# Kernel tuning notes

Hardware: AMD Instinct MI355X
Metric: run time of the kernel (lower is better)

Reference implementation:

```python
import jax, jax.numpy as jnp
import numpy as np

C = 1024
H = C // 64          # 16 heads
CH = 64              # head dim
NUM_BUCKETS = 32
MAX_DISTANCE = 64
REL_SCALE = float(np.sqrt(CH))  # (channels//num_heads)**0.5 = 8
EPS = 1e-5


def group_norm(x, gamma, beta, groups):
    # x: [B, C, T]
    B, Cc, T = x.shape
    xg = x.reshape(B, groups, -1)
    m = xg.mean(-1, keepdims=True)
    v = xg.var(-1, keepdims=True)
    xn = ((xg - m) * jax.lax.rsqrt(v + EPS)).reshape(B, Cc, T)
    return xn * gamma[None, :, None] + beta[None, :, None]


def conv1d(x, w, b, pad):
    # x: [B, Cin, T], w: [Cout, Cin, K]
    y = jax.lax.conv_general_dilated(x, w, (1,), [(pad, pad)],
                                     dimension_numbers=('NCH', 'OIH', 'NCH'))
    return y + b[None, :, None]


def rel_pos_bias(T, emb):
    # lucidrains RelativePositionBias, non-causal; emb: [num_buckets, H]
    pos = jnp.arange(T)
    n = pos[:, None] - pos[None, :]          # n = -(k - q) = q - k
    half = NUM_BUCKETS // 2                  # 16
    ret = (n < 0).astype(jnp.int32) * half
    n = jnp.abs(n)
    max_exact = half // 2                    # 8
    is_small = n < max_exact
    nf = jnp.maximum(n, 1).astype(jnp.float32)
    val_large = max_exact + (jnp.log(nf / max_exact)
                             / np.log(MAX_DISTANCE / max_exact)
                             * (half - max_exact)).astype(jnp.int32)
    val_large = jnp.minimum(val_large, half - 1)
    bucket = ret + jnp.where(is_small, n, val_large)  # [T, T]
    return emb[bucket].transpose(2, 0, 1)             # [H, T, T]


def setup_inputs() -> dict:
    key = jax.random.key(0)
    ks = jax.random.split(key, 20)
    B, T = 8, 1024
    s = 0.02
    return {
        'x': jax.random.normal(ks[0], (B, C, T), jnp.float32),
        # ResBlock in_layers
        'rb_gn1_g': jnp.ones((C,), jnp.float32),
        'rb_gn1_b': jnp.zeros((C,), jnp.float32),
        'rb_conv1_w': jax.random.normal(ks[1], (C, C, 3), jnp.float32) * s,
        'rb_conv1_b': jnp.zeros((C,), jnp.float32),
        # ResBlock out_layers (zero-init in original; randomized for testing)
        'rb_gn2_g': jnp.ones((C,), jnp.float32),
        'rb_gn2_b': jnp.zeros((C,), jnp.float32),
        'rb_conv2_w': jax.random.normal(ks[2], (C, C, 3), jnp.float32) * s,
        'rb_conv2_b': jnp.zeros((C,), jnp.float32),
        # outer GroupNorm(8, C)
        'norm_g': jnp.ones((C,), jnp.float32),
        'norm_b': jnp.zeros((C,), jnp.float32),
        # AttentionBlock
        'attn_gn_g': jnp.ones((C,), jnp.float32),
        'attn_gn_b': jnp.zeros((C,), jnp.float32),
        'qkv_w': jax.random.normal(ks[3], (3 * C, C, 1), jnp.float32) * s,
        'qkv_b': jnp.zeros((3 * C,), jnp.float32),
        'proj_w': jax.random.normal(ks[4], (C, C, 1), jnp.float32) * s,
        'proj_b': jnp.zeros((C,), jnp.float32),
        'rel_emb': jax.random.normal(ks[5], (NUM_BUCKETS, H), jnp.float32) * s,
    }


def reference(x, rb_gn1_g, rb_gn1_b, rb_conv1_w, rb_conv1_b,
              rb_gn2_g, rb_gn2_b, rb_conv2_w, rb_conv2_b,
              norm_g, norm_b, attn_gn_g, attn_gn_b,
              qkv_w, qkv_b, proj_w, proj_b, rel_emb):
    B, Cc, T = x.shape
    # ResBlock: GN32 -> SiLU -> conv3 -> GN32 -> SiLU -> (dropout=0) -> conv3, + skip
    h = jax.nn.silu(group_norm(x, rb_gn1_g, rb_gn1_b, 32))
    h = conv1d(h, rb_conv1_w, rb_conv1_b, 1)
    h = jax.nn.silu(group_norm(h, rb_gn2_g, rb_gn2_b, 32))
    h = conv1d(h, rb_conv2_w, rb_conv2_b, 1)
    h = x + h
    # outer GroupNorm(8)
    h = group_norm(h, norm_g, norm_b, 8)
    # AttentionBlock with relative position bias
    xin = h
    qkv = conv1d(group_norm(h, attn_gn_g, attn_gn_b, 32), qkv_w, qkv_b, 0)
    # channel layout after reshape(bs*H, 3*ch, T): [H, 3, ch]
    qkv = qkv.reshape(B, H, 3, CH, T)
    q, k, v = qkv[:, :, 0], qkv[:, :, 1], qkv[:, :, 2]
    scale = CH ** -0.25
    w = jnp.einsum('bhct,bhcs->bhts', q * scale, k * scale)
    bias = rel_pos_bias(T, rel_emb) * REL_SCALE       # [H, T, T]
    w = jax.nn.softmax((w + bias[None]).astype(jnp.float32), axis=-1).astype(w.dtype)
    a = jnp.einsum('bhts,bhcs->bhct', w, v).reshape(B, Cc, T)
    return xin + conv1d(a, proj_w, proj_b, 0)
```

## Files before the change

kernel.cpp:

```cpp
#include <hip/hip_runtime.h>

typedef __attribute__((ext_vector_type(4))) float f32x4;
typedef __attribute__((ext_vector_type(8))) __bf16 bf16x8;
typedef __attribute__((ext_vector_type(4))) unsigned short us4;
typedef __attribute__((ext_vector_type(8))) unsigned short us8;

#define DEVI static __device__ __forceinline__

DEVI unsigned short f2bf(float f){
  union { float f; unsigned u; } x; x.f = f;
  unsigned r = x.u + 0x7fffu + ((x.u >> 16) & 1u);
  return (unsigned short)(r >> 16);
}
DEVI float bf2f(unsigned short h){
  union { unsigned u; float f; } x; x.u = ((unsigned)h) << 16;
  return x.f;
}

typedef __attribute__((address_space(1))) unsigned int gu32;
typedef __attribute__((address_space(3))) unsigned int lu32;
DEVI void gll16(const void* g, void* l){
  __builtin_amdgcn_global_load_lds((gu32*)g, (lu32*)l, 16, 0, 0);
}

DEVI f32x4 mfma16(bf16x8 a, bf16x8 b, f32x4 c){
  return __builtin_amdgcn_mfma_f32_16x16x32_bf16(a, b, c, 0, 0, 0);
}

DEVI float wredsum(float v){
  #pragma unroll
  for (int m = 1; m < 64; m <<= 1) v += __shfl_xor(v, m);
  return v;
}

__global__ __launch_bounds__(256) void conv_w_prep(const float* __restrict__ w,
                                                   unsigned short* __restrict__ wp){
  int idx = blockIdx.x * 256 + threadIdx.x;
  const float* p = w + (size_t)idx * 3;
  wp[idx]           = f2bf(p[0]);
  wp[1048576 + idx] = f2bf(p[1]);
  wp[2097152 + idx] = f2bf(p[2]);
}

__global__ __launch_bounds__(256) void cast_f2b(const float* __restrict__ in,
                                                unsigned short* __restrict__ out, int n4){
  int idx = blockIdx.x * 256 + threadIdx.x;
  if (idx < n4){
    f32x4 v = *(const f32x4*)&in[(size_t)idx * 4];
    us4 o;
    #pragma unroll
    for (int j = 0; j < 4; j++) o[j] = f2bf(v[j]);
    *(us4*)&out[(size_t)idx * 4] = o;
  }
}

__global__ __launch_bounds__(256) void btab_k(const float* __restrict__ emb,
                                              float* __restrict__ btab){
  int idx = blockIdx.x * 256 + threadIdx.x;
  if (idx >= 2047 * 16) return;
  int d = idx >> 4, h = idx & 15;
  int n0 = d - 1023;
  int ret = (n0 < 0) ? 16 : 0;
  int n = (n0 < 0) ? -n0 : n0;
  int bucket;
  if (n < 8) bucket = ret + n;
  else {
    float ratio = logf((float)n * 0.125f) / 2.0794415416798357f;
    int vl = 8 + (int)(ratio * 8.0f);
    bucket = ret + (vl < 15 ? vl : 15);
  }
  btab[h * 2048 + d] = emb[bucket * 16 + h] * 11.541560327111707f;
}

__global__ __launch_bounds__(256) void zero_pads(unsigned short* __restrict__ h1p,
                                                 unsigned short* __restrict__ g2p){
  int idx = blockIdx.x * 256 + threadIdx.x;
  int b = idx >> 11, rr = (idx >> 10) & 1, c = idx & 1023;
  size_t off = ((size_t)b * 1026 + (rr ? 1025 : 0)) * 1024 + c;
  h1p[off] = 0; g2p[off] = 0;
}

__global__ __launch_bounds__(256) void gn_stats_cast(const float* __restrict__ in,
                                                     float2* __restrict__ st,
                                                     unsigned short* __restrict__ xb){
  const int g = blockIdx.x; const int tid = threadIdx.x;
  const float* p = in + (size_t)g * 32768;
  unsigned short* q = xb + (size_t)g * 32768;
  float s = 0.f, s2 = 0.f;
  for (int i = tid * 4; i < 32768; i += 1024){
    f32x4 v = *(const f32x4*)&p[i];
    us4 o;
    #pragma unroll
    for (int j = 0; j < 4; j++){ s += v[j]; s2 += v[j] * v[j]; o[j] = f2bf(v[j]); }
    *(us4*)&q[i] = o;
  }
  s = wredsum(s); s2 = wredsum(s2);
  __shared__ float rs[4], rs2[4];
  if ((tid & 63) == 0){ rs[tid >> 6] = s; rs2[tid >> 6] = s2; }
  __syncthreads();
  if (tid == 0){
    float S = rs[0] + rs[1] + rs[2] + rs[3];
    float S2 = rs2[0] + rs2[1] + rs2[2] + rs2[3];
    float m = S * (1.f / 32768.f);
    float var = S2 * (1.f / 32768.f) - m * m;
    st[g] = make_float2(m, rsqrtf(var + 1e-5f));
  }
}

template<int SILU, int INBF16, int OUTPAD, int FROMPART>
__global__ __launch_bounds__(256) void gn_apply_tr(
    const void* __restrict__ inp, const float2* __restrict__ st,
    const float* __restrict__ gma, const float* __restrict__ bta,
    unsigned short* __restrict__ out)
{
  const int gid = blockIdx.x;
  const int tc = gid & 15, g = (gid >> 4) & 31, b = gid >> 9;
  const int tid = threadIdx.x;
  const int t0 = tc * 64;
  __shared__ __align__(16) unsigned short tr[64 * 40];
  float2 s;
  if (FROMPART){
    int g8 = g >> 2, k = g & 3;
    float S = 0.f, S2 = 0.f;
    #pragma unroll
    for (int j = 0; j < 4; j++){
      float2 v = st[(size_t)(b * 8 + g8) * 16 + k * 4 + j];
      S += v.x; S2 += v.y;
    }
    float m = S * (1.f / 32768.f);
    float var = S2 * (1.f / 32768.f) - m * m;
    s = make_float2(m, rsqrtf(var + 1e-5f));
  } else {
    s = st[b * 32 + g];
  }
  int c = tid >> 3, t8 = (tid & 7) * 8;
  int ch = g * 32 + c;
  float sc = gma[ch] * s.y;
  float sh = bta[ch] - s.x * sc;
  float vv[8];
  if (INBF16){
    const unsigned short* p = (const unsigned short*)inp + ((size_t)b * 1024 + ch) * 1024 + t0 + t8;
    us8 v = *(const us8*)p;
    #pragma unroll
    for (int j = 0; j < 8; j++) vv[j] = bf2f(v[j]);
  } else {
    const float* p = (const float*)inp + ((size_t)b * 1024 + ch) * 1024 + t0 + t8;
    f32x4 v0 = *(const f32x4*)p; f32x4 v1 = *(const f32x4*)(p + 4);
    #pragma unroll
    for (int j = 0; j < 4; j++){ vv[j] = v0[j]; vv[4 + j] = v1[j]; }
  }
  #pragma unroll
  for (int j = 0; j < 8; j++){
    float v = vv[j] * sc + sh;
    if (SILU) v = v / (1.f + __expf(-v));
    tr[(t8 + j) * 40 + c] = f2bf(v);
  }
  __syncthreads();
  int t = tid >> 2, c8 = (tid & 3) * 8;
  us8 d = *(const us8*)&tr[t * 40 + c8];
  size_t row = OUTPAD ? ((size_t)b * 1026 + 1 + t0 + t) : ((size_t)b * 1024 + t0 + t);
  *(us8*)&out[row * 1024 + g * 32 + c8] = d;
}

template<int SILU>
__global__ __launch_bounds__(256) void gn2_apply(const unsigned short* __restrict__ c1,
    const float2* __restrict__ part2, const float* __restrict__ gma, const float* __restrict__ bta,
    unsigned short* __restrict__ outp)
{
  const int tid = threadIdx.x;
  const int ck = blockIdx.x & 31, b = blockIdx.x >> 5;
  const int g = tid >> 3;
  float S = 0.f, S2 = 0.f;
  #pragma unroll
  for (int tt = 0; tt < 8; tt++){
    float2 v = part2[(size_t)(b * 8 + tt) * 32 + g];
    S += v.x; S2 += v.y;
  }
  float mm = S * (1.f / 32768.f);
  float var = S2 * (1.f / 32768.f) - mm * mm;
  float2 s = make_float2(mm, rsqrtf(var + 1e-5f));
  float sc[4], sh[4];
  #pragma unroll
  for (int j = 0; j < 4; j++){ int ch = tid * 4 + j; sc[j] = gma[ch] * s.y; sh[j] = bta[ch] - s.x * sc[j]; }
  const unsigned short* p = c1 + ((size_t)b * 1024 + ck * 32) * 1024 + tid * 4;
  unsigned short* q = outp + ((size_t)b * 1026 + 1 + ck * 32) * 1024 + tid * 4;
  for (int r = 0; r < 32; r++){
    us4 v = *(const us4*)&p[(size_t)r * 1024];
    us4 o;
    #pragma unroll
    for (int j = 0; j < 4; j++){
      float f = bf2f(v[j]) * sc[j] + sh[j];
      if (SILU) f = f / (1.f + __expf(-f));
      o[j] = f2bf(f);
    }
    *(us4*)&q[(size_t)r * 1024] = o;
  }
}

__global__ __launch_bounds__(256) void gn8_apply(const unsigned short* __restrict__ r,
    const float2* __restrict__ part8, const float* __restrict__ gma, const float* __restrict__ bta,
    unsigned short* __restrict__ xin, float2* __restrict__ part32){
  const int gid = blockIdx.x; const int tid = threadIdx.x;
  const int sub = gid & 15, g = (gid >> 4) & 7, b = gid >> 7;
  float S = 0.f, S2 = 0.f;
  #pragma unroll
  for (int tt = 0; tt < 8; tt++){
    float2 v = part8[(size_t)(b * 8 + tt) * 8 + g];
    S += v.x; S2 += v.y;
  }
  float mm = S * (1.f / 131072.f);
  float var = S2 * (1.f / 131072.f) - mm * mm;
  float2 s = make_float2(mm, rsqrtf(var + 1e-5f));
  const unsigned short* pr = r + ((size_t)(b * 8 + g)) * 131072 + sub * 8192;
  unsigned short* px = xin + ((size_t)(b * 8 + g)) * 131072 + sub * 8192;
  float ps = 0.f, ps2 = 0.f;
  for (int i = tid * 8; i < 8192; i += 2048){
    int c = g * 128 + sub * 8 + (i >> 10);
    float sc = gma[c] * s.y, sh = bta[c] - s.x * sc;
    us8 v = *(const us8*)&pr[i];
    us8 o;
    #pragma unroll
    for (int j = 0; j < 8; j++){
      float f = bf2f(v[j]) * sc + sh;
      ps += f; ps2 += f * f;
      o[j] = f2bf(f);
    }
    *(us8*)&px[i] = o;
  }
  ps = wredsum(ps); ps2 = wredsum(ps2);
  __shared__ float rs[4], rs2[4];
  if ((tid & 63) == 0){ rs[tid >> 6] = ps; rs2[tid >> 6] = ps2; }
  __syncthreads();
  if (tid == 0)
    part32[(size_t)(b * 8 + g) * 16 + sub] =
      make_float2(rs[0] + rs[1] + rs[2] + rs[3], rs2[0] + rs2[1] + rs2[2] + rs2[3]);
}

template<int KK, int EPI, int GPART>
__global__ __launch_bounds__(256, 2) void gemm_k(
    const unsigned short* __restrict__ inT,
    const unsigned short* __restrict__ W,
    const float* __restrict__ bias,
    void* __restrict__ outp,
    void* __restrict__ resp,
    float2* __restrict__ part,
    int OC, int NT)
{
  __shared__ __align__(16) unsigned short Alds[2][128 * 64];
  __shared__ __align__(16) unsigned short Blds[2][128 * 64];
  __shared__ float sred[16];
  const int tid = threadIdx.x;
  const int lane = tid & 63;
  const int w = tid >> 6;
  const int wn = w >> 1, wo = w & 1;
  const int nt = blockIdx.x % NT;
  const int ot = blockIdx.x / NT;
  const int b = nt >> 3;
  const int t0 = (nt & 7) * 128;
  const int ob = ot * 128;
  const int rowbase = (KK == 3) ? (b * 1026 + t0) : (b * 1024 + t0);
  const int NTI = KK * 16;

  f32x4 acc[4][4];
  #pragma unroll
  for (int m = 0; m < 4; m++)
    #pragma unroll
    for (int n = 0; n < 4; n++) acc[m][n] = 0.f;

  const int lrow = lane >> 3;
  const int lblk = lane & 7;

  auto stage = [&](int kt, int bufsel){
    int kk = kt >> 4;
    int i0 = (kt & 15) * 64;
    const unsigned short* Ab = inT + (size_t)(rowbase + kk) * 1024;
    const unsigned short* Bb = W + ((size_t)kk * OC + ob) * 1024;
    #pragma unroll
    for (int j = 0; j < 4; ++j){
      int chunk = w * 4 + j;
      int row = chunk * 8 + lrow;
      int gcol = (lblk ^ (row & 7)) * 8;
      gll16(Ab + (size_t)row * 1024 + i0 + gcol, &Alds[bufsel][chunk * 512]);
      gll16(Bb + (size_t)row * 1024 + i0 + gcol, &Blds[bufsel][chunk * 512]);
    }
  };

  stage(0, 0);
  stage(1, 1);
  asm volatile("s_waitcnt vmcnt(8)" ::: "memory");
  __builtin_amdgcn_sched_barrier(0);
  __builtin_amdgcn_s_barrier();
  __builtin_amdgcn_sched_barrier(0);

  #pragma unroll 2
  for (int kt = 0; kt < NTI; ++kt){
    const int cur = kt & 1;
    const unsigned short* Ab = &Alds[cur][0];
    const unsigned short* Bb = &Blds[cur][0];
    bf16x8 af[2][4], bfv[2][4];
    #pragma unroll
    for (int m = 0; m < 4; m++){
      int row = wn * 64 + m * 16 + (lane & 15);
      #pragma unroll
      for (int k2 = 0; k2 < 2; k2++){
        int blk = ((lane >> 4) + k2 * 4) ^ (row & 7);
        af[k2][m] = *(const bf16x8*)&Ab[row * 64 + blk * 8];
      }
    }
    #pragma unroll
    for (int n = 0; n < 4; n++){
      int row = wo * 64 + n * 16 + (lane & 15);
      #pragma unroll
      for (int k2 = 0; k2 < 2; k2++){
        int blk = ((lane >> 4) + k2 * 4) ^ (row & 7);
        bfv[k2][n] = *(const bf16x8*)&Bb[row * 64 + blk * 8];
      }
    }
    asm volatile("s_waitcnt lgkmcnt(0)" ::: "memory");
    __builtin_amdgcn_sched_barrier(0);
    __builtin_amdgcn_s_barrier();
    __builtin_amdgcn_sched_barrier(0);
    if (kt + 2 < NTI) stage(kt + 2, cur);
    __builtin_amdgcn_sched_barrier(0);
    __builtin_amdgcn_s_setprio(1);
    #pragma unroll
    for (int k2 = 0; k2 < 2; k2++)
      #pragma unroll
      for (int m = 0; m < 4; m++)
        #pragma unroll
        for (int n = 0; n < 4; n++)
          acc[m][n] = mfma16(af[k2][m], bfv[k2][n], acc[m][n]);
    __builtin_amdgcn_s_setprio(0);
    __builtin_amdgcn_sched_barrier(0);
    if (kt + 2 < NTI){ asm volatile("s_waitcnt vmcnt(8)" ::: "memory"); }
    else             { asm volatile("s_waitcnt vmcnt(0)" ::: "memory"); }
    __builtin_amdgcn_sched_barrier(0);
    __builtin_amdgcn_s_barrier();
    __builtin_amdgcn_sched_barrier(0);
  }

  if (EPI == 0){
    unsigned short* out = (unsigned short*)outp;
    float ps[2] = {0.f, 0.f}, ps2[2] = {0.f, 0.f};
    #pragma unroll
    for (int m = 0; m < 4; m++){
      int tl = t0 + wn * 64 + m * 16 + ((lane >> 4) * 4);
      #pragma unroll
      for (int n = 0; n < 4; n++){
        int o = ob + wo * 64 + n * 16 + (lane & 15);
        float bz = bias[o];
        size_t base = ((size_t)b * 1024 + tl) * OC + o;
        #pragma unroll
        for (int r = 0; r < 4; r++){
          float v = acc[m][n][r] + bz;
          if (GPART == 2){ ps[n >> 1] += v; ps2[n >> 1] += v * v; }
          out[base + (size_t)r * OC] = f2bf(v);
        }
      }
    }
    if (GPART == 2){
      #pragma unroll
      for (int j = 0; j < 2; j++){ ps[j] = wredsum(ps[j]); ps2[j] = wredsum(ps2[j]); }
      if (lane == 0){
        sred[w * 4 + 0] = ps[0]; sred[w * 4 + 1] = ps2[0];
        sred[w * 4 + 2] = ps[1]; sred[w * 4 + 3] = ps2[1];
      }
      __syncthreads();
      if (tid < 4){
        int g = tid, woo = g >> 1, jj = g & 1;
        float S  = sred[woo * 4 + jj * 2 + 0] + sred[(woo + 2) * 4 + jj * 2 + 0];
        float S2 = sred[woo * 4 + jj * 2 + 1] + sred[(woo + 2) * 4 + jj * 2 + 1];
        part[(size_t)(b * 8 + (nt & 7)) * 32 + ot * 4 + g] = make_float2(S, S2);
      }
    }
  } else if (EPI == 3){
    unsigned short* qkT = (unsigned short*)outp;
    unsigned short* vT  = (unsigned short*)resp;
    #pragma unroll
    for (int m = 0; m < 4; m++){
      int tl = t0 + wn * 64 + m * 16 + ((lane >> 4) * 4);
      #pragma unroll
      for (int n = 0; n < 4; n++){
        int o0 = ob + wo * 64 + n * 16;
        int h = o0 / 192;
        int rem0 = o0 - h * 192;
        int o = o0 + (lane & 15);
        float bz = bias[o];
        if (rem0 < 128){
          size_t base = ((size_t)b * 1024 + tl) * 2048 + h * 128 + rem0 + (lane & 15);
          #pragma unroll
          for (int r = 0; r < 4; r++)
            qkT[base + (size_t)r * 2048] = f2bf(acc[m][n][r] + bz);
        } else {
          int c = rem0 - 128 + (lane & 15);
          size_t base = (((size_t)(b * 16 + h)) * 64 + c) * 1024 + tl;
          us4 o4;
          #pragma unroll
          for (int r = 0; r < 4; r++) o4[r] = f2bf(acc[m][n][r] + bz);
          *(us4*)&vT[base] = o4;
        }
      }
    }
  } else if (EPI == 4){
    unsigned short* out = (unsigned short*)outp;
    const unsigned short* xr = (const unsigned short*)resp;
    float ps = 0.f, ps2 = 0.f;
    #pragma unroll
    for (int m = 0; m < 4; m++){
      int tl = t0 + wn * 64 + m * 16 + ((lane >> 4) * 4);
      #pragma unroll
      for (int n = 0; n < 4; n++){
        int o = ob + wo * 64 + n * 16 + (lane & 15);
        float bz = bias[o];
        size_t base = ((size_t)b * 1024 + o) * 1024 + tl;
        us4 xv = *(const us4*)&xr[base];
        us4 ov;
        #pragma unroll
        for (int r = 0; r < 4; r++){
          float v = bf2f(xv[r]) + acc[m][n][r] + bz;
          if (GPART == 8){ ps += v; ps2 += v * v; }
          ov[r] = f2bf(v);
        }
        *(us4*)&out[base] = ov;
      }
    }
    if (GPART == 8){
      ps = wredsum(ps); ps2 = wredsum(ps2);
      if (lane == 0){ sred[w * 2] = ps; sred[w * 2 + 1] = ps2; }
      __syncthreads();
      if (tid == 0){
        float S = sred[0] + sred[2] + sred[4] + sred[6];
        float S2 = sred[1] + sred[3] + sred[5] + sred[7];
        part[(size_t)(b * 8 + (nt & 7)) * 8 + ot] = make_float2(S, S2);
      }
    }
  } else {
    float* out = (float*)outp;
    #pragma unroll
    for (int m = 0; m < 4; m++){
      int tl = t0 + wn * 64 + m * 16 + ((lane >> 4) * 4);
      #pragma unroll
      for (int n = 0; n < 4; n++){
        int o = ob + wo * 64 + n * 16 + (lane & 15);
        float bz = bias[o];
        size_t base = ((size_t)b * 1024 + o) * 1024 + tl;
        const unsigned short* xr = (const unsigned short*)resp;
        us4 xv = *(const us4*)&xr[base];
        f32x4 v;
        v[0] = bf2f(xv[0]); v[1] = bf2f(xv[1]); v[2] = bf2f(xv[2]); v[3] = bf2f(xv[3]);
        #pragma unroll
        for (int r = 0; r < 4; r++) v[r] += acc[m][n][r] + bz;
        *(f32x4*)&out[base] = v;
      }
    }
  }
}

__global__ __launch_bounds__(256, 3) void attn_k7(
    const unsigned short* __restrict__ qkT,
    const unsigned short* __restrict__ vT,
    const float* __restrict__ btab,
    unsigned short* __restrict__ aT)
{
  __shared__ __align__(16) unsigned short Kb[2][64 * 64];
  __shared__ __align__(16) unsigned short Vb[2][64 * 64];
  __shared__ __align__(16) unsigned short Pb[4][32 * 64];
  __shared__ __align__(16) float blds[1152];
  const int tid = threadIdx.x, lane = tid & 63, w = tid >> 6;
  const int d0 = blockIdx.x;
  const int xcd = d0 & 7, slot = d0 >> 3;
  const int bh = xcd * 16 + (slot >> 3);
  const int qt = slot & 7;
  const int h = bh & 15, b = bh >> 4;
  const int q0b = qt * 128;
  const int q0 = q0b + w * 32;
  const unsigned short* qk = qkT + (size_t)b * 1024 * 2048 + h * 128;
  const unsigned short* vh = vT + ((size_t)(b * 16 + h)) * 64 * 1024;
  const int lc = lane & 15, lg = lane >> 4;

  const float bneg = btab[h * 2048 + 0];
  const float bpos = btab[h * 2048 + 2046];

  for (int i = tid; i < 1151; i += 256)
    blds[i] = btab[h * 2048 + q0b + i];

  bf16x8 qf[2][2];
  #pragma unroll
  for (int m = 0; m < 2; m++){
    const unsigned short* qrow = qk + (size_t)(q0 + m * 16 + lc) * 2048;
    #pragma unroll
    for (int k2 = 0; k2 < 2; k2++)
      qf[m][k2] = *(const bf16x8*)&qrow[k2 * 32 + lg * 8];
  }
  float l_run[2];
  f32x4 oacc[2][4];
  l_run[0] = l_run[1] = 0.f;
  #pragma unroll
  for (int m = 0; m < 2; m++)
    #pragma unroll
    for (int cb = 0; cb < 4; cb++) oacc[m][cb] = 0.f;

  const int lr = lane >> 3, lb = lane & 7;
  const float qs = 0.18033688011112042f;

  #pragma unroll
  for (int j = 0; j < 2; j++){
    int chunk = w * 2 + j;
    int row = chunk * 8 + lr;
    int gcol = (lb ^ (row & 7)) * 8;
    gll16(qk + 64 + (size_t)row * 2048 + gcol, &Kb[0][chunk * 512]);
    gll16(vh + (size_t)row * 1024 + gcol, &Vb[0][chunk * 512]);
  }
  __syncthreads();

  for (int t = 0; t < 16; ++t){
    const int cur = t & 1;
    const int st0 = t * 64;
    if (t < 15){
      int nst = st0 + 64;
      #pragma unroll
      for (int j = 0; j < 2; j++){
        int chunk = w * 2 + j;
        int row = chunk * 8 + lr;
        int gcol = (lb ^ (row & 7)) * 8;
        gll16(qk + 64 + (size_t)(nst + row) * 2048 + gcol, &Kb[cur ^ 1][chunk * 512]);
        gll16(vh + (size_t)row * 1024 + nst + gcol, &Vb[cur ^ 1][chunk * 512]);
      }
    }
    f32x4 sfr[2][4];
    #pragma unroll
    for (int m = 0; m < 2; m++)
      #pragma unroll
      for (int sub = 0; sub < 4; sub++) sfr[m][sub] = 0.f;
    __builtin_amdgcn_s_setprio(1);
    #pragma unroll
    for (int sub = 0; sub < 4; sub++){
      int row = sub * 16 + lc;
      #pragma unroll
      for (int k2 = 0; k2 < 2; k2++){
        int blk = (lg + k2 * 4) ^ (row & 7);
        bf16x8 bk = *(const bf16x8*)&Kb[cur][row * 64 + blk * 8];
        sfr[0][sub] = mfma16(bk, qf[0][k2], sfr[0][sub]);
        sfr[1][sub] = mfma16(bk, qf[1][k2], sfr[1][sub]);
      }
    }
    __builtin_amdgcn_s_setprio(0);
    const bool unineg = (st0 >= q0 + 81);
    const bool unipos = (st0 + 113 <= q0);
    const bool uni = unineg || unipos;
    const float bc = unineg ? bneg : bpos;
    if (uni){
      #pragma unroll
      for (int m = 0; m < 2; m++){
        float ssum = 0.f;
        #pragma unroll
        for (int sub = 0; sub < 4; sub++)
          #pragma unroll
          for (int r = 0; r < 4; r++){
            float e = exp2f(fmaf(sfr[m][sub][r], qs, bc));
            sfr[m][sub][r] = e;
            ssum += e;
          }
        ssum += __shfl_xor(ssum, 16);
        ssum += __shfl_xor(ssum, 32);
        l_run[m] += ssum;
      }
    } else {
      #pragma unroll
      for (int m = 0; m < 2; m++){
        const float* bp = &blds[(w * 32 + m * 16 + lc) + 960 - st0];
        float ssum = 0.f;
        #pragma unroll
        for (int sub = 0; sub < 4; sub++){
          int off = 63 - sub * 16 - lg * 4;
          #pragma unroll
          for (int r = 0; r < 4; r++){
            float e = exp2f(fmaf(sfr[m][sub][r], qs, bp[off - r]));
            sfr[m][sub][r] = e;
            ssum += e;
          }
        }
        ssum += __shfl_xor(ssum, 16);
        ssum += __shfl_xor(ssum, 32);
        l_run[m] += ssum;
      }
    }
    unsigned short* P = &Pb[w][0];
    #pragma unroll
    for (int m = 0; m < 2; m++){
      int qrow = m * 16 + lc;
      int rsw = (qrow & 7) << 3;
      #pragma unroll
      for (int sub = 0; sub < 4; sub++){
        int col = sub * 16 + lg * 4;
        unsigned w0, w1;
        asm("v_cvt_pk_bf16_f32 %0, %1, %2" : "=v"(w0) : "v"(sfr[m][sub][0]), "v"(sfr[m][sub][1]));
        asm("v_cvt_pk_bf16_f32 %0, %1, %2" : "=v"(w1) : "v"(sfr[m][sub][2]), "v"(sfr[m][sub][3]));
        uint2 pk; pk.x = w0; pk.y = w1;
        *(uint2*)&P[qrow * 64 + (col ^ rsw)] = pk;
      }
    }
    __builtin_amdgcn_s_setprio(1);
    #pragma unroll
    for (int k2 = 0; k2 < 2; k2++){
      bf16x8 pa[2];
      #pragma unroll
      for (int m = 0; m < 2; m++){
        int rowp = m * 16 + lc;
        int blkp = (lg + k2 * 4) ^ (rowp & 7);
        pa[m] = *(const bf16x8*)&P[rowp * 64 + blkp * 8];
      }
      #pragma unroll
      for (int cb = 0; cb < 4; cb++){
        int ch = cb * 16 + lc;
        int blkv = (lg + k2 * 4) ^ (ch & 7);
        bf16x8 bv = *(const bf16x8*)&Vb[cur][ch * 64 + blkv * 8];
        oacc[0][cb] = mfma16(pa[0], bv, oacc[0][cb]);
        oacc[1][cb] = mfma16(pa[1], bv, oacc[1][cb]);
      }
    }
    __builtin_amdgcn_s_setprio(0);
    __syncthreads();
  }
  #pragma unroll
  for (int m = 0; m < 2; m++)
    #pragma unroll
    for (int r = 0; r < 4; r++){
      float li = 1.0f / __shfl(l_run[m], lg * 4 + r);
      int tq = q0 + m * 16 + lg * 4 + r;
      #pragma unroll
      for (int cb = 0; cb < 4; cb++){
        int ch = h * 64 + cb * 16 + lc;
        aT[((size_t)b * 1024 + tq) * 1024 + ch] = f2bf(oacc[m][cb][r] * li);
      }
    }
}

extern "C" void kernel_launch(void* const* d_in, const int* in_sizes, int n_in,
                              void* d_out, int out_size, void* d_ws, size_t ws_size,
                              hipStream_t stream)
{
  const float* x       = (const float*)d_in[0];
  const float* gn1_g   = (const float*)d_in[1];
  const float* gn1_b   = (const float*)d_in[2];
  const float* conv1_w = (const float*)d_in[3];
  const float* conv1_b = (const float*)d_in[4];
  const float* gn2_g   = (const float*)d_in[5];
  const float* gn2_b   = (const float*)d_in[6];
  const float* conv2_w = (const float*)d_in[7];
  const float* conv2_b = (const float*)d_in[8];
  const float* norm_g  = (const float*)d_in[9];
  const float* norm_b  = (const float*)d_in[10];
  const float* agn_g   = (const float*)d_in[11];
  const float* agn_b   = (const float*)d_in[12];
  const float* qkv_w   = (const float*)d_in[13];
  const float* qkv_b   = (const float*)d_in[14];
  const float* proj_w  = (const float*)d_in[15];
  const float* proj_b  = (const float*)d_in[16];
  const float* rel_emb = (const float*)d_in[17];

  if (ws_size < 139526144u) return;

  char* ws = (char*)d_ws;
  unsigned short* w1p   = (unsigned short*)(ws + 0);
  unsigned short* w2p   = (unsigned short*)(ws + 6291456);
  unsigned short* wqkv  = (unsigned short*)(ws + 12582912);
  unsigned short* wproj = (unsigned short*)(ws + 18874368);
  float* btab           = (float*)(ws + 20971520);
  float2* stats1        = (float2*)(ws + 21102592);
  float2* part2n        = (float2*)(ws + 21110784);
  float2* part8n        = (float2*)(ws + 21127168);
  float2* part32        = (float2*)(ws + 21131264);
  unsigned short* h1p   = (unsigned short*)(ws + 22020096);
  unsigned short* c1    = (unsigned short*)(ws + 38830080);
  unsigned short* g2p   = (unsigned short*)(ws + 55607296);
  unsigned short* qkT   = h1p;
  unsigned short* vT    = (unsigned short*)(ws + 55574528);
  unsigned short* xb    = (unsigned short*)(ws + 72417280);
  unsigned short* attn_in = (unsigned short*)(ws + 72417280);
  unsigned short* xin   = (unsigned short*)(ws + 105971712);
  unsigned short* aT    = (unsigned short*)(ws + 122748928);

  conv_w_prep<<<4096, 256, 0, stream>>>(conv1_w, w1p);
  conv_w_prep<<<4096, 256, 0, stream>>>(conv2_w, w2p);
  cast_f2b<<<3072, 256, 0, stream>>>(qkv_w, wqkv, 3072 * 1024 / 4);
  cast_f2b<<<1024, 256, 0, stream>>>(proj_w, wproj, 1024 * 1024 / 4);
  btab_k<<<128, 256, 0, stream>>>(rel_emb, btab);
  zero_pads<<<64, 256, 0, stream>>>(h1p, g2p);

  gn_stats_cast<<<256, 256, 0, stream>>>(x, stats1, xb);
  gn_apply_tr<1, 1, 1, 0><<<4096, 256, 0, stream>>>(xb, stats1, gn1_g, gn1_b, h1p);

  gemm_k<3, 0, 2><<<512, 256, 0, stream>>>(h1p, w1p, conv1_b, c1, nullptr, part2n, 1024, 64);
  gn2_apply<1><<<256, 256, 0, stream>>>(c1, part2n, gn2_g, gn2_b, g2p);

  gemm_k<3, 4, 8><<<512, 256, 0, stream>>>(g2p, w2p, conv2_b, xb, xb, part8n, 1024, 64);
  gn8_apply<<<1024, 256, 0, stream>>>(xb, part8n, norm_g, norm_b, xin, part32);

  gn_apply_tr<0, 1, 0, 1><<<4096, 256, 0, stream>>>(xin, part32, agn_g, agn_b, attn_in);

  gemm_k<1, 3, 0><<<1536, 256, 0, stream>>>(attn_in, wqkv, qkv_b, qkT, vT, nullptr, 3072, 64);

  attn_k7<<<1024, 256, 0, stream>>>(qkT, vT, btab, aT);

  gemm_k<1, 2, 0><<<512, 256, 0, stream>>>(aT, wproj, proj_b, d_out, xin, nullptr, 1024, 64);
}
```

Before: 347.2 us.

## Halve attention query tile per block and compute softmax row sums via MFMA

The attention kernel now processes 64 queries per block (16 per wave) instead of 128, doubling the grid to 2048 blocks. The row-sum of exponentials is computed by an extra MFMA against a ones vector instead of per-lane adds and cross-lane shuffles. This is meant to raise parallelism and occupancy and to take reduction work off the VALU. In exchange, every K/V tile is now loaded and staged through LDS twice as many times per query. The row sums are also accumulated from the bf16-rounded probabilities rather than the fp32 values.

```diff
diff --git a/kernel.cpp b/kernel.cpp
--- a/kernel.cpp
+++ b/kernel.cpp
@@ -456,7 +456,7 @@
   }
 }
 
-__global__ __launch_bounds__(256, 3) void attn_k7(
+__global__ __launch_bounds__(256, 3) void attn_k8(
     const unsigned short* __restrict__ qkT,
     const unsigned short* __restrict__ vT,
     const float* __restrict__ btab,
@@ -464,16 +464,16 @@
 {
   __shared__ __align__(16) unsigned short Kb[2][64 * 64];
   __shared__ __align__(16) unsigned short Vb[2][64 * 64];
-  __shared__ __align__(16) unsigned short Pb[4][32 * 64];
-  __shared__ __align__(16) float blds[1152];
+  __shared__ __align__(16) unsigned short Pb[4][16 * 64];
+  __shared__ __align__(16) float blds[1088];
   const int tid = threadIdx.x, lane = tid & 63, w = tid >> 6;
   const int d0 = blockIdx.x;
   const int xcd = d0 & 7, slot = d0 >> 3;
-  const int bh = xcd * 16 + (slot >> 3);
-  const int qt = slot & 7;
+  const int bh = xcd * 16 + (slot >> 4);
+  const int qt = slot & 15;
   const int h = bh & 15, b = bh >> 4;
-  const int q0b = qt * 128;
-  const int q0 = q0b + w * 32;
+  const int q0b = qt * 64;
+  const int q0 = q0b + w * 16;
   const unsigned short* qk = qkT + (size_t)b * 1024 * 2048 + h * 128;
   const unsigned short* vh = vT + ((size_t)(b * 16 + h)) * 64 * 1024;
   const int lc = lane & 15, lg = lane >> 4;
@@ -481,24 +481,27 @@
   const float bneg = btab[h * 2048 + 0];
   const float bpos = btab[h * 2048 + 2046];
 
-  for (int i = tid; i < 1151; i += 256)
+  for (int i = tid; i < 1087; i += 256)
     blds[i] = btab[h * 2048 + q0b + i];
 
-  bf16x8 qf[2][2];
-  #pragma unroll
-  for (int m = 0; m < 2; m++){
-    const unsigned short* qrow = qk + (size_t)(q0 + m * 16 + lc) * 2048;
+  bf16x8 qf[2];
+  {
+    const unsigned short* qrow = qk + (size_t)(q0 + lc) * 2048;
     #pragma unroll
     for (int k2 = 0; k2 < 2; k2++)
-      qf[m][k2] = *(const bf16x8*)&qrow[k2 * 32 + lg * 8];
-  }
-  float l_run[2];
-  f32x4 oacc[2][4];
-  l_run[0] = l_run[1] = 0.f;
-  #pragma unroll
-  for (int m = 0; m < 2; m++)
-    #pragma unroll
-    for (int cb = 0; cb < 4; cb++) oacc[m][cb] = 0.f;
+      qf[k2] = *(const bf16x8*)&qrow[k2 * 32 + lg * 8];
+  }
+  bf16x8 onesf;
+  {
+    us8 u;
+    #pragma unroll
+    for (int j = 0; j < 8; j++) u[j] = 0x3F80;
+    onesf = *(bf16x8*)&u;
+  }
+  f32x4 oacc[4], lacc;
+  #pragma unroll
+  for (int cb = 0; cb < 4; cb++) oacc[cb] = 0.f;
+  lacc = 0.f;
 
   const int lr = lane >> 3, lb = lane & 7;
   const float qs = 0.18033688011112042f;
@@ -527,11 +530,9 @@
         gll16(vh + (size_t)row * 1024 + nst + gcol, &Vb[cur ^ 1][chunk * 512]);
       }
     }
-    f32x4 sfr[2][4];
-    #pragma unroll
-    for (int m = 0; m < 2; m++)
-      #pragma unroll
-      for (int sub = 0; sub < 4; sub++) sfr[m][sub] = 0.f;
+    f32x4 sfr[4];
+    #pragma unroll
+    for (int sub = 0; sub < 4; sub++) sfr[sub] = 0.f;
     __builtin_amdgcn_s_setprio(1);
     #pragma unroll
     for (int sub = 0; sub < 4; sub++){
@@ -540,100 +541,69 @@
       for (int k2 = 0; k2 < 2; k2++){
         int blk = (lg + k2 * 4) ^ (row & 7);
         bf16x8 bk = *(const bf16x8*)&Kb[cur][row * 64 + blk * 8];
-        sfr[0][sub] = mfma16(bk, qf[0][k2], sfr[0][sub]);
-        sfr[1][sub] = mfma16(bk, qf[1][k2], sfr[1][sub]);
+        sfr[sub] = mfma16(bk, qf[k2], sfr[sub]);
       }
     }
     __builtin_amdgcn_s_setprio(0);
-    const bool unineg = (st0 >= q0 + 81);
+    const bool unineg = (st0 >= q0 + 65);
     const bool unipos = (st0 + 113 <= q0);
-    const bool uni = unineg || unipos;
-    const float bc = unineg ? bneg : bpos;
-    if (uni){
-      #pragma unroll
-      for (int m = 0; m < 2; m++){
-        float ssum = 0.f;
+    if (unineg || unipos){
+      const float bc = unineg ? bneg : bpos;
+      #pragma unroll
+      for (int sub = 0; sub < 4; sub++)
         #pragma unroll
-        for (int sub = 0; sub < 4; sub++)
-          #pragma unroll
-          for (int r = 0; r < 4; r++){
-            float e = exp2f(fmaf(sfr[m][sub][r], qs, bc));
-            sfr[m][sub][r] = e;
-            ssum += e;
-          }
-        ssum += __shfl_xor(ssum, 16);
-        ssum += __shfl_xor(ssum, 32);
-        l_run[m] += ssum;
-      }
+        for (int r = 0; r < 4; r++)
+          sfr[sub][r] = exp2f(fmaf(sfr[sub][r], qs, bc));
     } else {
-      #pragma unroll
-      for (int m = 0; m < 2; m++){
-        const float* bp = &blds[(w * 32 + m * 16 + lc) + 960 - st0];
-        float ssum = 0.f;
+      const float* bp = &blds[(w * 16 + lc) + 960 - st0];
+      #pragma unroll
+      for (int sub = 0; sub < 4; sub++){
+        int off = 63 - sub * 16 - lg * 4;
         #pragma unroll
-        for (int sub = 0; sub < 4; sub++){
-          int off = 63 - sub * 16 - lg * 4;
-          #pragma unroll
-          for (int r = 0; r < 4; r++){
-            float e = exp2f(fmaf(sfr[m][sub][r], qs, bp[off - r]));
-            sfr[m][sub][r] = e;
-            ssum += e;
-          }
-        }
-        ssum += __shfl_xor(ssum, 16);
-        ssum += __shfl_xor(ssum, 32);
-        l_run[m] += ssum;
+        for (int r = 0; r < 4; r++)
+          sfr[sub][r] = exp2f(fmaf(sfr[sub][r], qs, bp[off - r]));
       }
     }
     unsigned short* P = &Pb[w][0];
-    #pragma unroll
-    for (int m = 0; m < 2; m++){
-      int qrow = m * 16 + lc;
-      int rsw = (qrow & 7) << 3;
+    {
+      int rsw = (lc & 7) << 3;
       #pragma unroll
       for (int sub = 0; sub < 4; sub++){
         int col = sub * 16 + lg * 4;
         unsigned w0, w1;
-        asm("v_cvt_pk_bf16_f32 %0, %1, %2" : "=v"(w0) : "v"(sfr[m][sub][0]), "v"(sfr[m][sub][1]));
-        asm("v_cvt_pk_bf16_f32 %0, %1, %2" : "=v"(w1) : "v"(sfr[m][sub][2]), "v"(sfr[m][sub][3]));
+        asm("v_cvt_pk_bf16_f32 %0, %1, %2" : "=v"(w0) : "v"(sfr[sub][0]), "v"(sfr[sub][1]));
+        asm("v_cvt_pk_bf16_f32 %0, %1, %2" : "=v"(w1) : "v"(sfr[sub][2]), "v"(sfr[sub][3]));
         uint2 pk; pk.x = w0; pk.y = w1;
-        *(uint2*)&P[qrow * 64 + (col ^ rsw)] = pk;
+        *(uint2*)&P[lc * 64 + (col ^ rsw)] = pk;
       }
     }
     __builtin_amdgcn_s_setprio(1);
     #pragma unroll
     for (int k2 = 0; k2 < 2; k2++){
-      bf16x8 pa[2];
-      #pragma unroll
-      for (int m = 0; m < 2; m++){
-        int rowp = m * 16 + lc;
-        int blkp = (lg + k2 * 4) ^ (rowp & 7);
-        pa[m] = *(const bf16x8*)&P[rowp * 64 + blkp * 8];
-      }
+      int blkp = (lg + k2 * 4) ^ (lc & 7);
+      bf16x8 pa = *(const bf16x8*)&P[lc * 64 + blkp * 8];
       #pragma unroll
       for (int cb = 0; cb < 4; cb++){
         int ch = cb * 16 + lc;
         int blkv = (lg + k2 * 4) ^ (ch & 7);
         bf16x8 bv = *(const bf16x8*)&Vb[cur][ch * 64 + blkv * 8];
-        oacc[0][cb] = mfma16(pa[0], bv, oacc[0][cb]);
-        oacc[1][cb] = mfma16(pa[1], bv, oacc[1][cb]);
-      }
+        oacc[cb] = mfma16(pa, bv, oacc[cb]);
+      }
+      lacc = mfma16(pa, onesf, lacc);
     }
     __builtin_amdgcn_s_setprio(0);
     __syncthreads();
   }
   #pragma unroll
-  for (int m = 0; m < 2; m++)
-    #pragma unroll
-    for (int r = 0; r < 4; r++){
-      float li = 1.0f / __shfl(l_run[m], lg * 4 + r);
-      int tq = q0 + m * 16 + lg * 4 + r;
-      #pragma unroll
-      for (int cb = 0; cb < 4; cb++){
-        int ch = h * 64 + cb * 16 + lc;
-        aT[((size_t)b * 1024 + tq) * 1024 + ch] = f2bf(oacc[m][cb][r] * li);
-      }
-    }
+  for (int r = 0; r < 4; r++){
+    float li = 1.0f / lacc[r];
+    int tq = q0 + lg * 4 + r;
+    #pragma unroll
+    for (int cb = 0; cb < 4; cb++){
+      int ch = h * 64 + cb * 16 + lc;
+      aT[((size_t)b * 1024 + tq) * 1024 + ch] = f2bf(oacc[cb][r] * li);
+    }
+  }
 }
 
 extern "C" void kernel_launch(void* const* d_in, const int* in_sizes, int n_in,
@@ -701,7 +671,7 @@
 
   gemm_k<1, 3, 0><<<1536, 256, 0, stream>>>(attn_in, wqkv, qkv_b, qkT, vT, nullptr, 3072, 64);
 
-  attn_k7<<<1024, 256, 0, stream>>>(qkT, vT, btab, aT);
+  attn_k8<<<2048, 256, 0, stream>>>(qkT, vT, btab, aT);
 
   gemm_k<1, 2, 0><<<512, 256, 0, stream>>>(aT, wproj, proj_b, d_out, xin, nullptr, 1024, 64);
 }
```

Measured after the change: 350.9 us. About the same (+1.1%).
